# Kernel tuning notes

Hardware: AMD Instinct MI355X
Metric: run time of the kernel (lower is better)

## Reference

```python
import jax, jax.numpy as jnp
import numpy as np

IMG = 512
STRIDES = (8, 16, 32, 64, 128)
AREAS = np.array([(IMG // s) ** 2 for s in STRIDES])  # [4096,1024,256,64,16]
A_TOTAL = int(AREAS.sum())  # 5456
LEVELS = 5
TOP_K = 3
MAX_OBJ = 32
NUM_CLASSES = 80
BATCH = 16


def _detections():
    # [LEVELS, A_TOTAL] one-hot level membership per anchor (tf.pad of ones)
    det = np.zeros((LEVELS, A_TOTAL), np.float32)
    off = 0
    for i, a in enumerate(AREAS):
        det[i, off:off + a] = 1.0
        off += a
    return jnp.asarray(det)


def focal_loss(y_true, y_pred, alpha=0.25, gamma=2.0):
    # y_pred are sigmoid probabilities; sum over classes -> [B, A]
    p = jnp.clip(y_pred, 1e-7, 1.0 - 1e-7)
    ce = -(y_true * jnp.log(p) + (1.0 - y_true) * jnp.log(1.0 - p))
    alpha_t = y_true * alpha + (1.0 - y_true) * (1.0 - alpha)
    pt = y_true * (1.0 - p) + (1.0 - y_true) * p
    return jnp.sum(alpha_t * pt ** gamma * ce, axis=-1)


def giou_loss(y_true, y_pred):
    # ltrb distance encoding (all >= 0) -> per-anchor GIoU loss [B, A]
    tl, tt, tr, tb = (y_true[..., i] for i in range(4))
    pl, pt_, pr, pb = (y_pred[..., i] for i in range(4))
    area_t = (tl + tr) * (tt + tb)
    area_p = (pl + pr) * (pt_ + pb)
    inter = (jnp.minimum(tl, pl) + jnp.minimum(tr, pr)) * (jnp.minimum(tt, pt_) + jnp.minimum(tb, pb))
    union = area_t + area_p - inter
    iou = inter / jnp.maximum(union, 1e-7)
    enc = (jnp.maximum(tl, pl) + jnp.maximum(tr, pr)) * (jnp.maximum(tt, pt_) + jnp.maximum(tb, pb))
    giou = iou - (enc - union) / jnp.maximum(enc, 1e-7)
    return 1.0 - giou


def dwlm(total_loss, ind, bbox_cnt):
    # total_loss [B,A], ind [B,A] int, bbox_cnt [B] int
    det = _detections()                                   # [L, A]
    obj_ids = jnp.arange(MAX_OBJ)                         # [O]
    valid = obj_ids[None, :] < bbox_cnt[:, None]          # [B, O]
    obj_mask = (ind[:, None, :] == obj_ids[None, :, None]).astype(total_loss.dtype)  # [B,O,A]
    det_mask = obj_mask[:, :, None, :] * det[None, None]  # [B,O,L,A]
    obj_l_sum = jnp.einsum('ba,bola->bol', total_loss, det_mask)
    cnt = jnp.sum(det_mask, axis=-1)                      # [B,O,L]
    mean = obj_l_sum / jnp.maximum(1.0, cnt)
    lmax = jnp.max(mean, axis=-1, keepdims=True) + 1e-5
    mean = jnp.where(mean == 0.0, lmax, mean)
    lmin = jnp.min(mean, axis=-1, keepdims=True)
    target = 1.0 - (mean - lmin) / (lmax - lmin)          # [B,O,L]
    kth = jax.lax.top_k(target, TOP_K)[0][..., -1:]
    target = jnp.where(target >= kth, target, 0.0)
    target = jnp.where(valid[..., None], target, 0.0)     # drop padded objects
    return jnp.einsum('bol,bola->ba', target, det_mask)   # scatter-sum back to anchors


def setup_inputs() -> dict:
    key = jax.random.key(0)
    k = jax.random.split(key, 6)
    return {
        'cls_pred': jax.random.uniform(k[0], (BATCH, A_TOTAL, NUM_CLASSES), jnp.float32),
        'loc_pred': jax.random.uniform(k[1], (BATCH, A_TOTAL, 4), jnp.float32),
        'cls_tar': jax.random.uniform(k[2], (BATCH, A_TOTAL, NUM_CLASSES + 2), jnp.float32),
        'loc_tar': jax.random.uniform(k[3], (BATCH, A_TOTAL, 4), jnp.float32),
        'ind_tar': jax.random.randint(k[4], (BATCH, A_TOTAL, 1), 0, MAX_OBJ, jnp.int32),
        'bboxes_cnt': jax.random.randint(k[5], (BATCH, 1), 0, MAX_OBJ, jnp.int32),
    }


def reference(cls_pred, loc_pred, cls_tar, loc_tar, ind_tar, bboxes_cnt):
    cls_loss = focal_loss(cls_tar[..., :-2], cls_pred)
    loc_loss = giou_loss(loc_tar, loc_pred)
    dwlm_out = dwlm(cls_loss + loc_loss, ind_tar[..., 0], bboxes_cnt[..., 0])
    pos_mask = cls_tar[..., -1]
    dwlm_out_masked = jnp.where(pos_mask > 0.0, dwlm_out, 1.0)
    return dwlm_out_masked[..., None], pos_mask
```

## Files before the change

kernel.cpp:

```cpp
#include <hip/hip_runtime.h>

constexpr int A_TOTAL = 5456;
constexpr int BATCH = 16;
constexpr int NUM_CLASSES = 80;
constexpr int NUM_CH = NUM_CLASSES + 2;
constexpr int MAX_OBJ = 32;
constexpr int LEVELS = 5;
constexpr int BINS = MAX_OBJ * LEVELS;
constexpr int BLK_L = 1024;
constexpr int APB = BLK_L / 4;
constexpr int NBLK = (A_TOTAL + APB - 1) / APB;
constexpr int BLK_G = 256;

__device__ __forceinline__ int lev_of(int a) {
    return (a < 4096) ? 0 : (a < 5120) ? 1 : (a < 5376) ? 2 : (a < 5440) ? 3 : 4;
}

__global__ void __launch_bounds__(BLK_L)
loss_accum_kernel(const float* __restrict__ cls_pred,
                  const float* __restrict__ loc_pred,
                  const float* __restrict__ cls_tar,
                  const float* __restrict__ loc_tar,
                  const int*   __restrict__ ind_tar,
                  float* __restrict__ p_sum,
                  float* __restrict__ p_cnt,
                  float* __restrict__ out) {
    __shared__ float s_sum[BINS];
    __shared__ float s_cnt[BINS];
    const int t = threadIdx.x;
    if (t < BINS) { s_sum[t] = 0.f; s_cnt[t] = 0.f; }
    __syncthreads();

    const int b = blockIdx.y;
    const int a = blockIdx.x * APB + (t >> 2);
    const int q = t & 3;
    const bool valid = a < A_TOTAL;

    float fl = 0.f;
    size_t row = 0;
    if (valid) {
        row = (size_t)b * A_TOTAL + a;
        const float4* pred4 = (const float4*)cls_pred + row * 20 + q;
        const float2* tar2  = (const float2*)cls_tar  + row * 41 + 2 * q;
        #pragma unroll
        for (int j = 0; j < 5; ++j) {
            float4 p4 = pred4[4 * j];
            float2 ta = tar2[8 * j];
            float2 tb = tar2[8 * j + 1];
            float ps[4] = {p4.x, p4.y, p4.z, p4.w};
            float ts[4] = {ta.x, ta.y, tb.x, tb.y};
            #pragma unroll
            for (int k = 0; k < 4; ++k) {
                float p  = fminf(fmaxf(ps[k], 1e-7f), 1.0f - 1e-7f);
                float tt = ts[k];
                float ce = -(tt * __logf(p) + (1.f - tt) * __logf(1.f - p));
                float alpha_t = tt * 0.25f + (1.f - tt) * 0.75f;
                float pt = tt * (1.f - p) + (1.f - tt) * p;
                fl += alpha_t * pt * pt * ce;
            }
        }
    }
    fl += __shfl_xor(fl, 1);
    fl += __shfl_xor(fl, 2);

    if (valid && q == 0) {
        float pos = cls_tar[row * NUM_CH + (NUM_CH - 1)];
        out[(size_t)BATCH * A_TOTAL + row] = pos;

        float4 T = ((const float4*)(loc_tar  + row * 4))[0];
        float4 P = ((const float4*)(loc_pred + row * 4))[0];
        float area_t = (T.x + T.z) * (T.y + T.w);
        float area_p = (P.x + P.z) * (P.y + P.w);
        float inter  = (fminf(T.x, P.x) + fminf(T.z, P.z)) * (fminf(T.y, P.y) + fminf(T.w, P.w));
        float uni    = area_t + area_p - inter;
        float iou    = inter / fmaxf(uni, 1e-7f);
        float enc    = (fmaxf(T.x, P.x) + fmaxf(T.z, P.z)) * (fmaxf(T.y, P.y) + fmaxf(T.w, P.w));
        float giou   = iou - (enc - uni) / fmaxf(enc, 1e-7f);
        float loss   = fl + (1.f - giou);

        int bin = ind_tar[row] * LEVELS + lev_of(a);
        atomicAdd(&s_sum[bin], loss);
        atomicAdd(&s_cnt[bin], 1.0f);
    }
    __syncthreads();
    const size_t slot = ((size_t)b * NBLK + blockIdx.x) * BINS;
    if (t < BINS) {
        p_sum[slot + t] = s_sum[t];
        p_cnt[slot + t] = s_cnt[t];
    }
}

__global__ void __launch_bounds__(BLK_G)
gather_kernel(const float* __restrict__ p_sum,
              const float* __restrict__ p_cnt,
              const int*   __restrict__ ind_tar,
              const int*   __restrict__ bbox_cnt,
              float* __restrict__ out) {
    __shared__ float s_mean[BINS];
    __shared__ float s_tgt[BINS];
    const int t = threadIdx.x;
    const int b = blockIdx.y;

    if (t < BINS) {
        float s = 0.f, c = 0.f;
        const size_t base = (size_t)b * NBLK * BINS + t;
        #pragma unroll
        for (int k = 0; k < NBLK; ++k) {
            s += p_sum[base + (size_t)k * BINS];
            c += p_cnt[base + (size_t)k * BINS];
        }
        s_mean[t] = s / fmaxf(1.0f, c);
    }
    __syncthreads();

    if (t < MAX_OBJ) {
        float mean[LEVELS];
        float mx = -1e30f;
        #pragma unroll
        for (int l = 0; l < LEVELS; ++l) {
            mean[l] = s_mean[t * LEVELS + l];
            mx = fmaxf(mx, mean[l]);
        }
        float lmax = mx + 1e-5f;
        float mn = 1e30f;
        #pragma unroll
        for (int l = 0; l < LEVELS; ++l) {
            if (mean[l] == 0.0f) mean[l] = lmax;
            mn = fminf(mn, mean[l]);
        }
        float denom = lmax - mn;
        float tgt[LEVELS];
        float m1 = -1e30f, m2 = -1e30f, m3 = -1e30f;
        #pragma unroll
        for (int l = 0; l < LEVELS; ++l) {
            float v = 1.0f - (mean[l] - mn) / denom;
            tgt[l] = v;
            if (v > m1)      { m3 = m2; m2 = m1; m1 = v; }
            else if (v > m2) { m3 = m2; m2 = v; }
            else if (v > m3) { m3 = v; }
        }
        const bool valid = t < bbox_cnt[b];
        #pragma unroll
        for (int l = 0; l < LEVELS; ++l) {
            float v = tgt[l];
            v = (v >= m3) ? v : 0.0f;
            s_tgt[t * LEVELS + l] = valid ? v : 0.0f;
        }
    }
    __syncthreads();

    const int a = blockIdx.x * BLK_G + t;
    if (a >= A_TOTAL) return;
    const size_t row = (size_t)b * A_TOTAL + a;
    float pos = out[(size_t)BATCH * A_TOTAL + row];
    int o = ind_tar[row];
    out[row] = (pos > 0.0f) ? s_tgt[o * LEVELS + lev_of(a)] : 1.0f;
}

extern "C" void kernel_launch(void* const* d_in, const int* in_sizes, int n_in,
                              void* d_out, int out_size, void* d_ws, size_t ws_size,
                              hipStream_t stream) {
    const float* cls_pred = (const float*)d_in[0];
    const float* loc_pred = (const float*)d_in[1];
    const float* cls_tar  = (const float*)d_in[2];
    const float* loc_tar  = (const float*)d_in[3];
    const int*   ind_tar  = (const int*)d_in[4];
    const int*   bbox_cnt = (const int*)d_in[5];
    float* out = (float*)d_out;

    float* p_sum = (float*)d_ws;
    float* p_cnt = p_sum + (size_t)BATCH * NBLK * BINS;

    loss_accum_kernel<<<dim3(NBLK, BATCH), dim3(BLK_L), 0, stream>>>(
        cls_pred, loc_pred, cls_tar, loc_tar, ind_tar, p_sum, p_cnt, out);
    gather_kernel<<<dim3((A_TOTAL + BLK_G - 1) / BLK_G, BATCH), dim3(BLK_G), 0, stream>>>(
        p_sum, p_cnt, ind_tar, bbox_cnt, out);
}
```

Baseline: 23.49 us.

## Shrink loss blocks to 256 threads and accumulate bins via global atomics

The loss-accumulation kernel now uses 256-thread blocks (64 anchors each), which gives about four times as many blocks for better occupancy and load balance. The per-block partial-sum arrays are replaced by global atomicAdd into a single per-batch set of bins, skipping bins that received no anchors. The gather kernel therefore reads one value per bin instead of looping over every block's partials. A memset of the workspace is added before the launch, and the bin sums become order-nondeterministic because of float atomics.

```diff
diff --git a/kernel.cpp b/kernel.cpp
--- a/kernel.cpp
+++ b/kernel.cpp
@@ -7,23 +7,23 @@
 constexpr int MAX_OBJ = 32;
 constexpr int LEVELS = 5;
 constexpr int BINS = MAX_OBJ * LEVELS;
-constexpr int BLK_L = 1024;
-constexpr int APB = BLK_L / 4;
-constexpr int NBLK = (A_TOTAL + APB - 1) / APB;
-constexpr int BLK_G = 256;
+constexpr int BLK = 256;
+constexpr int APB = BLK / 4;
+constexpr int NBLK_L = (A_TOTAL + APB - 1) / APB;
+constexpr int NBLK_G = (A_TOTAL + BLK - 1) / BLK;
 
 __device__ __forceinline__ int lev_of(int a) {
     return (a < 4096) ? 0 : (a < 5120) ? 1 : (a < 5376) ? 2 : (a < 5440) ? 3 : 4;
 }
 
-__global__ void __launch_bounds__(BLK_L)
+__global__ void __launch_bounds__(BLK, 8)
 loss_accum_kernel(const float* __restrict__ cls_pred,
                   const float* __restrict__ loc_pred,
                   const float* __restrict__ cls_tar,
                   const float* __restrict__ loc_tar,
                   const int*   __restrict__ ind_tar,
-                  float* __restrict__ p_sum,
-                  float* __restrict__ p_cnt,
+                  float* __restrict__ g_sum,
+                  float* __restrict__ g_cnt,
                   float* __restrict__ out) {
     __shared__ float s_sum[BINS];
     __shared__ float s_cnt[BINS];
@@ -83,16 +83,18 @@
         atomicAdd(&s_cnt[bin], 1.0f);
     }
     __syncthreads();
-    const size_t slot = ((size_t)b * NBLK + blockIdx.x) * BINS;
     if (t < BINS) {
-        p_sum[slot + t] = s_sum[t];
-        p_cnt[slot + t] = s_cnt[t];
+        float c = s_cnt[t];
+        if (c != 0.f) {
+            atomicAdd(&g_sum[b * BINS + t], s_sum[t]);
+            atomicAdd(&g_cnt[b * BINS + t], c);
+        }
     }
 }
 
-__global__ void __launch_bounds__(BLK_G)
-gather_kernel(const float* __restrict__ p_sum,
-              const float* __restrict__ p_cnt,
+__global__ void __launch_bounds__(BLK)
+gather_kernel(const float* __restrict__ g_sum,
+              const float* __restrict__ g_cnt,
               const int*   __restrict__ ind_tar,
               const int*   __restrict__ bbox_cnt,
               float* __restrict__ out) {
@@ -102,13 +104,8 @@
     const int b = blockIdx.y;
 
     if (t < BINS) {
-        float s = 0.f, c = 0.f;
-        const size_t base = (size_t)b * NBLK * BINS + t;
-        #pragma unroll
-        for (int k = 0; k < NBLK; ++k) {
-            s += p_sum[base + (size_t)k * BINS];
-            c += p_cnt[base + (size_t)k * BINS];
-        }
+        float s = g_sum[b * BINS + t];
+        float c = g_cnt[b * BINS + t];
         s_mean[t] = s / fmaxf(1.0f, c);
     }
     __syncthreads();
@@ -149,7 +146,7 @@
     }
     __syncthreads();
 
-    const int a = blockIdx.x * BLK_G + t;
+    const int a = blockIdx.x * BLK + t;
     if (a >= A_TOTAL) return;
     const size_t row = (size_t)b * A_TOTAL + a;
     float pos = out[(size_t)BATCH * A_TOTAL + row];
@@ -168,11 +165,13 @@
     const int*   bbox_cnt = (const int*)d_in[5];
     float* out = (float*)d_out;
 
-    float* p_sum = (float*)d_ws;
-    float* p_cnt = p_sum + (size_t)BATCH * NBLK * BINS;
+    float* g_sum = (float*)d_ws;
+    float* g_cnt = g_sum + (size_t)BATCH * BINS;
 
-    loss_accum_kernel<<<dim3(NBLK, BATCH), dim3(BLK_L), 0, stream>>>(
-        cls_pred, loc_pred, cls_tar, loc_tar, ind_tar, p_sum, p_cnt, out);
-    gather_kernel<<<dim3((A_TOTAL + BLK_G - 1) / BLK_G, BATCH), dim3(BLK_G), 0, stream>>>(
-        p_sum, p_cnt, ind_tar, bbox_cnt, out);
+    hipMemsetAsync(d_ws, 0, 2 * BATCH * BINS * sizeof(float), stream);
+
+    loss_accum_kernel<<<dim3(NBLK_L, BATCH), dim3(BLK), 0, stream>>>(
+        cls_pred, loc_pred, cls_tar, loc_tar, ind_tar, g_sum, g_cnt, out);
+    gather_kernel<<<dim3(NBLK_G, BATCH), dim3(BLK), 0, stream>>>(
+        g_sum, g_cnt, ind_tar, bbox_cnt, out);
 }
```

Measured after the change: 28.46 us. 1.21x slower.
